# Optimization experiments

Measured on AMD Instinct MI355X. Metric: run time of the kernel, lower is better.

Reference implementation:

```python
import jax, jax.numpy as jnp
import numpy as np

LAMBDA = 0.7
RATIO = 3
EPS = 1e-6


def setup_inputs() -> dict:
    key = jax.random.key(0)
    k1, k2, k3 = jax.random.split(key, 3)
    bs, n, w, h = 8, 7, 640, 640
    preds = jax.random.normal(k1, (bs, n, w, h), dtype=jnp.float32)
    labels = jax.random.randint(k2, (bs, n, w, h), 0, 2, dtype=jnp.int32)
    training_mask = jax.random.randint(k3, (bs, w, h), 0, 2, dtype=jnp.int32)
    return {"preds": preds, "labels": labels, "training_mask": training_mask}


def _dice(S, G):
    # S, G: [C, P]; per-channel dice coefficient, then mean over channels
    num = 2.0 * jnp.sum(S * G, axis=-1)
    den = jnp.sum(S * S, axis=-1) + jnp.sum(G * G, axis=-1) + EPS
    return jnp.mean(num / den)


def _single_sample(pred, label, mask):
    # pred, label: [n, P]; mask: [P]
    P = pred.shape[-1]
    p = jax.nn.sigmoid(pred)
    pred_n = p[-1] * mask            # masked full-text prediction
    label_n = label[-1] * mask

    # --- OHEM mask M (cal_M): keep all positives + top (ratio*n_pos) hardest negatives ---
    pos = pred_n >= 0.5
    n_pos = jnp.sum(pos)
    n_neg_all = jnp.sum(~pos)
    k = n_pos * RATIO
    # sigmoid outputs are in (0,1); sentinel -1 pushes positives to the end of the descending sort
    neg_vals = jnp.where(pos, -1.0, pred_n)
    sorted_desc = -jnp.sort(-neg_vals)
    thr = sorted_desc[jnp.clip(k - 1, 0, P - 1)]  # k-th largest negative score
    ohem_active = (n_neg_all > k) & (k > 0)
    M = jnp.where(ohem_active, (pred_n >= thr).astype(jnp.float32), 1.0)

    # L_c: dice loss on OHEM-selected full-text map
    L_c = 1.0 - _dice((pred_n * M)[None, :], (label_n * M)[None, :])

    # L_s: dice loss on shrunk kernels, gated by predicted text region W
    W = (pred_n >= 0.5).astype(jnp.float32)
    L_s = 1.0 - _dice(p[:-1] * W, label[:-1] * W)

    loss = LAMBDA * L_c + (1.0 - LAMBDA) * L_s
    return L_c, L_s, loss


def reference(preds, labels, training_mask):
    bs, n, w, h = preds.shape
    preds = preds.reshape(bs, n, w * h)
    labels = labels.reshape(bs, n, w * h).astype(jnp.float32)
    mask = training_mask.reshape(bs, w * h).astype(jnp.float32)
    L_c, L_s, loss = jax.vmap(_single_sample)(preds, labels, mask)
    # reduction='mean'
    return L_c.mean(), L_s.mean(), loss.mean()
```

## Files before the change

### kernel.cpp

```cpp
#include <hip/hip_runtime.h>

#define BS   8
#define NCH  7
#define PX   409600
#define NBIN 65536
#define WIN_LO 0x3000u
#define WIN_SZ 4096
#define EPSF 1e-6f

__device__ __forceinline__ float sigf(float x) {
    return 1.0f / (1.0f + __expf(-x));
}

__device__ __forceinline__ unsigned wred_u(unsigned v) {
    #pragma unroll
    for (int o = 32; o; o >>= 1) v += __shfl_down(v, o);
    return v;
}

__device__ __forceinline__ float wred_f(float v) {
    #pragma unroll
    for (int o = 32; o; o >>= 1) v += __shfl_down(v, o);
    return v;
}

__global__ __launch_bounds__(256) void k_hist(const float* __restrict__ preds,
                                              const int* __restrict__ mask,
                                              unsigned* __restrict__ hist1,
                                              unsigned* __restrict__ n_pos) {
    int b = blockIdx.y;
    const float* pr = preds + ((size_t)b * NCH + 6) * PX;
    const int* mk = mask + (size_t)b * PX;
    __shared__ unsigned lh[WIN_SZ];
    for (int j = threadIdx.x; j < WIN_SZ; j += blockDim.x) lh[j] = 0u;
    __syncthreads();
    unsigned pos_cnt = 0, zero_cnt = 0;
    for (int i = blockIdx.x * blockDim.x + threadIdx.x; i < PX; i += gridDim.x * blockDim.x) {
        float pn = sigf(pr[i]) * (float)mk[i];
        if (pn >= 0.5f) {
            pos_cnt++;
        } else {
            unsigned bits = __float_as_uint(pn);
            if (bits == 0u) {
                zero_cnt++;
            } else {
                unsigned hb = bits >> 16;
                if (hb >= WIN_LO && hb < WIN_LO + WIN_SZ)
                    atomicAdd(&lh[hb - WIN_LO], 1u);
                else
                    atomicAdd(&hist1[(size_t)b * NBIN + hb], 1u);
            }
        }
    }
    __syncthreads();
    for (int j = threadIdx.x; j < WIN_SZ; j += blockDim.x) {
        unsigned c = lh[j];
        if (c) atomicAdd(&hist1[(size_t)b * NBIN + WIN_LO + j], c);
    }
    __shared__ unsigned ws2[2][4];
    unsigned pv = wred_u(pos_cnt), zv = wred_u(zero_cnt);
    int lane = threadIdx.x & 63, wid = threadIdx.x >> 6;
    if (lane == 0) { ws2[0][wid] = pv; ws2[1][wid] = zv; }
    __syncthreads();
    if (threadIdx.x == 0) {
        unsigned pt = 0, zt = 0;
        #pragma unroll
        for (int w = 0; w < 4; w++) { pt += ws2[0][w]; zt += ws2[1][w]; }
        if (pt) atomicAdd(&n_pos[b], pt);
        if (zt) atomicAdd(&hist1[(size_t)b * NBIN], zt);
    }
}

__device__ void select_bin(const unsigned* __restrict__ h, unsigned k,
                           unsigned* out_bin, unsigned* out_rank) {
    __shared__ unsigned cs[256];
    __shared__ unsigned sel_chunk, sel_rem;
    int t = threadIdx.x;
    unsigned s = 0;
    const unsigned* hp = h + t * 256;
    #pragma unroll 8
    for (int j = 0; j < 256; j++) s += hp[j];
    cs[t] = s;
    __syncthreads();
    #pragma unroll
    for (int off = 1; off < 256; off <<= 1) {
        unsigned v = cs[t];
        unsigned a = (t + off < 256) ? cs[t + off] : 0u;
        __syncthreads();
        cs[t] = v + a;
        __syncthreads();
    }
    {
        unsigned sfx  = cs[t];
        unsigned sfx1 = (t < 255) ? cs[t + 1] : 0u;
        if (sfx >= k && sfx1 < k) { sel_chunk = (unsigned)t; sel_rem = k - sfx1; }
    }
    __syncthreads();
    unsigned chunk = sel_chunk, krem = sel_rem;
    cs[t] = h[chunk * 256 + t];
    __syncthreads();
    #pragma unroll
    for (int off = 1; off < 256; off <<= 1) {
        unsigned v = cs[t];
        unsigned a = (t + off < 256) ? cs[t + off] : 0u;
        __syncthreads();
        cs[t] = v + a;
        __syncthreads();
    }
    {
        unsigned sfx  = cs[t];
        unsigned sfx1 = (t < 255) ? cs[t + 1] : 0u;
        if (sfx >= krem && sfx1 < krem) {
            *out_bin  = chunk * 256 + (unsigned)t;
            *out_rank = krem - sfx1;
        }
    }
    __syncthreads();
}

__global__ __launch_bounds__(256) void k_find_hi(const unsigned* __restrict__ hist1,
                                                 const unsigned* __restrict__ n_pos,
                                                 unsigned* __restrict__ hi_bin,
                                                 unsigned* __restrict__ rankv,
                                                 unsigned* __restrict__ activev,
                                                 float* __restrict__ thr) {
    int b = blockIdx.x;
    unsigned np_ = n_pos[b];
    unsigned k = np_ * 3u;
    unsigned nneg = (unsigned)PX - np_;
    if (!(nneg > k && k > 0u)) {
        if (threadIdx.x == 0) { activev[b] = 0u; thr[b] = -1.0f; }
        return;
    }
    __shared__ unsigned rb, rr;
    select_bin(hist1 + (size_t)b * NBIN, k, &rb, &rr);
    if (threadIdx.x == 0) {
        activev[b] = 1u;
        hi_bin[b] = rb;
        rankv[b] = rr;
        if (rb == 0u) thr[b] = 0.0f;
    }
}

__global__ __launch_bounds__(256) void k_refine(const float* __restrict__ preds,
                                                const int* __restrict__ mask,
                                                const unsigned* __restrict__ hi_bin,
                                                const unsigned* __restrict__ activev,
                                                unsigned* __restrict__ hist2) {
    int b = blockIdx.y;
    if (!activev[b]) return;
    unsigned hi = hi_bin[b];
    if (hi == 0u) return;
    const float* pr = preds + ((size_t)b * NCH + 6) * PX;
    const int* mk = mask + (size_t)b * PX;
    unsigned* h2 = hist2 + (size_t)b * NBIN;
    for (int i = blockIdx.x * blockDim.x + threadIdx.x; i < PX; i += gridDim.x * blockDim.x) {
        float pn = sigf(pr[i]) * (float)mk[i];
        if (pn < 0.5f) {
            unsigned bits = __float_as_uint(pn);
            if ((bits >> 16) == hi) atomicAdd(&h2[bits & 0xFFFFu], 1u);
        }
    }
}

__global__ __launch_bounds__(256) void k_find_lo(const unsigned* __restrict__ hist2,
                                                 const unsigned* __restrict__ hi_bin,
                                                 const unsigned* __restrict__ rankv,
                                                 const unsigned* __restrict__ activev,
                                                 float* __restrict__ thr) {
    int b = blockIdx.x;
    if (!activev[b]) return;
    unsigned hi = hi_bin[b];
    if (hi == 0u) return;
    __shared__ unsigned rb, rr;
    select_bin(hist2 + (size_t)b * NBIN, rankv[b], &rb, &rr);
    if (threadIdx.x == 0) thr[b] = __uint_as_float((hi << 16) | rb);
}

__global__ __launch_bounds__(256) void k_sums(const float* __restrict__ preds,
                                              const int* __restrict__ labels,
                                              const int* __restrict__ mask,
                                              const float* __restrict__ thr,
                                              float* __restrict__ sums) {
    int b = blockIdx.y;
    const float* pr = preds + (size_t)b * NCH * PX;
    const int* lb = labels + (size_t)b * NCH * PX;
    const int* mk = mask + (size_t)b * PX;
    float thr_b = thr[b];

    float a0 = 0.f, a1 = 0.f, a2 = 0.f;
    float sn[6] = {0.f, 0.f, 0.f, 0.f, 0.f, 0.f};
    float sp[6] = {0.f, 0.f, 0.f, 0.f, 0.f, 0.f};
    float sl[6] = {0.f, 0.f, 0.f, 0.f, 0.f, 0.f};

    for (int i = blockIdx.x * blockDim.x + threadIdx.x; i < PX; i += gridDim.x * blockDim.x) {
        float m  = (float)mk[i];
        float p6 = sigf(pr[6 * PX + i]);
        float pn = p6 * m;
        float Mi = (pn >= thr_b) ? 1.0f : 0.0f;
        float ln = (float)lb[6 * PX + i] * m;
        a0 += pn * ln * Mi;
        a1 += pn * pn * Mi;
        a2 += ln * Mi;
        float W = (pn >= 0.5f) ? 1.0f : 0.0f;
        #pragma unroll
        for (int c = 0; c < 6; c++) {
            float pc = sigf(pr[c * PX + i]);
            float lc = (float)lb[c * PX + i];
            sn[c] += pc * lc * W;
            sp[c] += pc * pc * W;
            sl[c] += lc * W;
        }
    }

    float vals[21];
    vals[0] = a0; vals[1] = a1; vals[2] = a2;
    #pragma unroll
    for (int c = 0; c < 6; c++) { vals[3 + c] = sn[c]; vals[9 + c] = sp[c]; vals[15 + c] = sl[c]; }

    __shared__ float red[4][21];
    int lane = threadIdx.x & 63, wid = threadIdx.x >> 6;
    #pragma unroll
    for (int j = 0; j < 21; j++) {
        float v = wred_f(vals[j]);
        if (lane == 0) red[wid][j] = v;
    }
    __syncthreads();
    if (threadIdx.x < 21) {
        float tot = red[0][threadIdx.x] + red[1][threadIdx.x] + red[2][threadIdx.x] + red[3][threadIdx.x];
        atomicAdd(&sums[b * 21 + threadIdx.x], tot);
    }
}

__global__ void k_final(const float* __restrict__ sums, float* __restrict__ out) {
    int t = threadIdx.x;
    float Lc = 0.f, Ls = 0.f;
    if (t < BS) {
        const float* s = sums + t * 21;
        Lc = 1.0f - (2.0f * s[0]) / (s[1] + s[2] + EPSF);
        float acc = 0.f;
        #pragma unroll
        for (int c = 0; c < 6; c++)
            acc += (2.0f * s[3 + c]) / (s[9 + c] + s[15 + c] + EPSF);
        Ls = 1.0f - acc * (1.0f / 6.0f);
    }
    #pragma unroll
    for (int o = 4; o; o >>= 1) { Lc += __shfl_down(Lc, o); Ls += __shfl_down(Ls, o); }
    if (t == 0) {
        float lc_m = Lc * (1.0f / (float)BS);
        float ls_m = Ls * (1.0f / (float)BS);
        out[0] = lc_m;
        out[1] = ls_m;
        out[2] = 0.7f * lc_m + 0.3f * ls_m;
    }
}

extern "C" void kernel_launch(void* const* d_in, const int* in_sizes, int n_in,
                              void* d_out, int out_size, void* d_ws, size_t ws_size,
                              hipStream_t stream) {
    const float* preds = (const float*)d_in[0];
    const int* labels  = (const int*)d_in[1];
    const int* mask    = (const int*)d_in[2];
    float* out = (float*)d_out;

    unsigned* hist1   = (unsigned*)d_ws;
    unsigned* hist2   = hist1 + (size_t)BS * NBIN;
    unsigned* n_pos   = hist2 + (size_t)BS * NBIN;
    unsigned* hi_bin  = n_pos + BS;
    unsigned* rankv   = hi_bin + BS;
    unsigned* activev = rankv + BS;
    float*    thr     = (float*)(activev + BS);
    float*    sums    = thr + BS;

    size_t zero_words = (size_t)2 * BS * NBIN + 5 * BS + (size_t)BS * 21;
    hipMemsetAsync(d_ws, 0, zero_words * sizeof(unsigned), stream);

    dim3 g1(80, BS);
    hipLaunchKernelGGL(k_hist, g1, dim3(256), 0, stream, preds, mask, hist1, n_pos);

    hipLaunchKernelGGL(k_find_hi, dim3(BS), dim3(256), 0, stream,
                       hist1, n_pos, hi_bin, rankv, activev, thr);

    dim3 g3(40, BS);
    hipLaunchKernelGGL(k_refine, g3, dim3(256), 0, stream,
                       preds, mask, hi_bin, activev, hist2);

    hipLaunchKernelGGL(k_find_lo, dim3(BS), dim3(256), 0, stream,
                       hist2, hi_bin, rankv, activev, thr);

    dim3 g5(160, BS);
    hipLaunchKernelGGL(k_sums, g5, dim3(256), 0, stream,
                       preds, labels, mask, thr, sums);

    hipLaunchKernelGGL(k_final, dim3(1), dim3(64), 0, stream, sums, out);
}
```

Measured before the change: 250.5 us.

## Fuse kernel-channel dice sums into histogram pass and add chunk-level histogram summaries

Moves the six shrunk-kernel dice accumulations, which depend only on the W>=0.5 gate, into the first histogram pass. The final pass then only reads channel 6 to apply the OHEM threshold, so the large 6-channel read no longer has to wait for threshold selection. Also keeps per-256-bin chunk counters so the select step skips the 64K-bin scan, and vectorises loads with float4/int4. The cost is extra global atomics for chunk counters in the histogram and refine passes.

```diff
diff --git a/kernel.cpp b/kernel.cpp
--- a/kernel.cpp
+++ b/kernel.cpp
@@ -4,6 +4,7 @@
 #define NCH  7
 #define PX   409600
 #define NBIN 65536
+#define NCHK 256
 #define WIN_LO 0x3000u
 #define WIN_SZ 4096
 #define EPSF 1e-6f
@@ -24,39 +25,94 @@
     return v;
 }
 
-__global__ __launch_bounds__(256) void k_hist(const float* __restrict__ preds,
+__global__ __launch_bounds__(256) void k_main(const float* __restrict__ preds,
+                                              const int* __restrict__ labels,
                                               const int* __restrict__ mask,
                                               unsigned* __restrict__ hist1,
-                                              unsigned* __restrict__ n_pos) {
+                                              unsigned* __restrict__ chunks1,
+                                              unsigned* __restrict__ n_pos,
+                                              float* __restrict__ sums) {
     int b = blockIdx.y;
-    const float* pr = preds + ((size_t)b * NCH + 6) * PX;
-    const int* mk = mask + (size_t)b * PX;
+    const float* pr = preds + (size_t)b * NCH * PX;
+    const int*   lb = labels + (size_t)b * NCH * PX;
+    const int*   mk = mask + (size_t)b * PX;
+
     __shared__ unsigned lh[WIN_SZ];
-    for (int j = threadIdx.x; j < WIN_SZ; j += blockDim.x) lh[j] = 0u;
-    __syncthreads();
+    for (int j = threadIdx.x; j < WIN_SZ; j += 256) lh[j] = 0u;
+    __syncthreads();
+
     unsigned pos_cnt = 0, zero_cnt = 0;
-    for (int i = blockIdx.x * blockDim.x + threadIdx.x; i < PX; i += gridDim.x * blockDim.x) {
-        float pn = sigf(pr[i]) * (float)mk[i];
-        if (pn >= 0.5f) {
-            pos_cnt++;
-        } else {
-            unsigned bits = __float_as_uint(pn);
-            if (bits == 0u) {
-                zero_cnt++;
+    float acc[18];
+    #pragma unroll
+    for (int j = 0; j < 18; j++) acc[j] = 0.f;
+
+    for (int g = blockIdx.x * 256 + threadIdx.x; g < PX / 4; g += gridDim.x * 256) {
+        int px = g * 4;
+        float4 p6 = *(const float4*)(pr + 6 * PX + px);
+        int4   m4 = *(const int4*)(mk + px);
+        float mm[4]  = {(float)m4.x, (float)m4.y, (float)m4.z, (float)m4.w};
+        float p6a[4] = {p6.x, p6.y, p6.z, p6.w};
+        float W[4];
+        #pragma unroll
+        for (int u = 0; u < 4; u++) {
+            float pn = sigf(p6a[u]) * mm[u];
+            if (pn >= 0.5f) {
+                pos_cnt++; W[u] = 1.0f;
             } else {
-                unsigned hb = bits >> 16;
-                if (hb >= WIN_LO && hb < WIN_LO + WIN_SZ)
-                    atomicAdd(&lh[hb - WIN_LO], 1u);
-                else
-                    atomicAdd(&hist1[(size_t)b * NBIN + hb], 1u);
+                W[u] = 0.0f;
+                unsigned bits = __float_as_uint(pn);
+                if (bits == 0u) {
+                    zero_cnt++;
+                } else {
+                    unsigned hb = bits >> 16;
+                    if (hb - WIN_LO < WIN_SZ) {
+                        atomicAdd(&lh[hb - WIN_LO], 1u);
+                    } else {
+                        atomicAdd(&hist1[(size_t)b * NBIN + hb], 1u);
+                        atomicAdd(&chunks1[b * NCHK + (hb >> 8)], 1u);
+                    }
+                }
             }
         }
-    }
-    __syncthreads();
-    for (int j = threadIdx.x; j < WIN_SZ; j += blockDim.x) {
+        #pragma unroll
+        for (int c = 0; c < 6; c++) {
+            float4 pc4 = *(const float4*)(pr + c * PX + px);
+            int4   lc4 = *(const int4*)(lb + c * PX + px);
+            float pcs[4] = {pc4.x, pc4.y, pc4.z, pc4.w};
+            float lcs[4] = {(float)lc4.x, (float)lc4.y, (float)lc4.z, (float)lc4.w};
+            #pragma unroll
+            for (int u = 0; u < 4; u++) {
+                float s = sigf(pcs[u]);
+                float l = lcs[u];
+                acc[c]      += s * l * W[u];
+                acc[6 + c]  += s * s * W[u];
+                acc[12 + c] += l * W[u];
+            }
+        }
+    }
+    __syncthreads();
+
+    for (int j = threadIdx.x; j < WIN_SZ; j += 256) {
         unsigned c = lh[j];
         if (c) atomicAdd(&hist1[(size_t)b * NBIN + WIN_LO + j], c);
     }
+    __shared__ unsigned csum[256];
+    {
+        unsigned s = 0;
+        int chunk = threadIdx.x >> 4, part = threadIdx.x & 15;
+        const unsigned* base = &lh[chunk * 256 + part * 16];
+        #pragma unroll
+        for (int j = 0; j < 16; j++) s += base[j];
+        csum[threadIdx.x] = s;
+    }
+    __syncthreads();
+    if (threadIdx.x < 16) {
+        unsigned s = 0;
+        #pragma unroll
+        for (int j = 0; j < 16; j++) s += csum[threadIdx.x * 16 + j];
+        if (s) atomicAdd(&chunks1[b * NCHK + 48 + threadIdx.x], s);
+    }
+
     __shared__ unsigned ws2[2][4];
     unsigned pv = wred_u(pos_cnt), zv = wred_u(zero_cnt);
     int lane = threadIdx.x & 63, wid = threadIdx.x >> 6;
@@ -67,20 +123,33 @@
         #pragma unroll
         for (int w = 0; w < 4; w++) { pt += ws2[0][w]; zt += ws2[1][w]; }
         if (pt) atomicAdd(&n_pos[b], pt);
-        if (zt) atomicAdd(&hist1[(size_t)b * NBIN], zt);
-    }
-}
-
-__device__ void select_bin(const unsigned* __restrict__ h, unsigned k,
-                           unsigned* out_bin, unsigned* out_rank) {
+        if (zt) {
+            atomicAdd(&hist1[(size_t)b * NBIN], zt);
+            atomicAdd(&chunks1[b * NCHK], zt);
+        }
+    }
+
+    __shared__ float red[4][18];
+    #pragma unroll
+    for (int j = 0; j < 18; j++) {
+        float v = wred_f(acc[j]);
+        if (lane == 0) red[wid][j] = v;
+    }
+    __syncthreads();
+    if (threadIdx.x < 18) {
+        float tot = red[0][threadIdx.x] + red[1][threadIdx.x] +
+                    red[2][threadIdx.x] + red[3][threadIdx.x];
+        atomicAdd(&sums[b * 21 + 3 + threadIdx.x], tot);
+    }
+}
+
+__device__ void select2(const unsigned* __restrict__ chunks,
+                        const unsigned* __restrict__ bins,
+                        unsigned k, unsigned* out_bin, unsigned* out_rank) {
     __shared__ unsigned cs[256];
-    __shared__ unsigned sel_chunk, sel_rem;
+    __shared__ unsigned sel_c, sel_r;
     int t = threadIdx.x;
-    unsigned s = 0;
-    const unsigned* hp = h + t * 256;
-    #pragma unroll 8
-    for (int j = 0; j < 256; j++) s += hp[j];
-    cs[t] = s;
+    cs[t] = chunks[t];
     __syncthreads();
     #pragma unroll
     for (int off = 1; off < 256; off <<= 1) {
@@ -93,11 +162,11 @@
     {
         unsigned sfx  = cs[t];
         unsigned sfx1 = (t < 255) ? cs[t + 1] : 0u;
-        if (sfx >= k && sfx1 < k) { sel_chunk = (unsigned)t; sel_rem = k - sfx1; }
-    }
-    __syncthreads();
-    unsigned chunk = sel_chunk, krem = sel_rem;
-    cs[t] = h[chunk * 256 + t];
+        if (sfx >= k && sfx1 < k) { sel_c = (unsigned)t; sel_r = k - sfx1; }
+    }
+    __syncthreads();
+    unsigned chunk = sel_c, krem = sel_r;
+    cs[t] = bins[chunk * 256 + t];
     __syncthreads();
     #pragma unroll
     for (int off = 1; off < 256; off <<= 1) {
@@ -119,6 +188,7 @@
 }
 
 __global__ __launch_bounds__(256) void k_find_hi(const unsigned* __restrict__ hist1,
+                                                 const unsigned* __restrict__ chunks1,
                                                  const unsigned* __restrict__ n_pos,
                                                  unsigned* __restrict__ hi_bin,
                                                  unsigned* __restrict__ rankv,
@@ -133,7 +203,7 @@
         return;
     }
     __shared__ unsigned rb, rr;
-    select_bin(hist1 + (size_t)b * NBIN, k, &rb, &rr);
+    select2(chunks1 + b * NCHK, hist1 + (size_t)b * NBIN, k, &rb, &rr);
     if (threadIdx.x == 0) {
         activev[b] = 1u;
         hi_bin[b] = rb;
@@ -146,7 +216,8 @@
                                                 const int* __restrict__ mask,
                                                 const unsigned* __restrict__ hi_bin,
                                                 const unsigned* __restrict__ activev,
-                                                unsigned* __restrict__ hist2) {
+                                                unsigned* __restrict__ hist2,
+                                                unsigned* __restrict__ chunks2) {
     int b = blockIdx.y;
     if (!activev[b]) return;
     unsigned hi = hi_bin[b];
@@ -154,16 +225,30 @@
     const float* pr = preds + ((size_t)b * NCH + 6) * PX;
     const int* mk = mask + (size_t)b * PX;
     unsigned* h2 = hist2 + (size_t)b * NBIN;
-    for (int i = blockIdx.x * blockDim.x + threadIdx.x; i < PX; i += gridDim.x * blockDim.x) {
-        float pn = sigf(pr[i]) * (float)mk[i];
-        if (pn < 0.5f) {
-            unsigned bits = __float_as_uint(pn);
-            if ((bits >> 16) == hi) atomicAdd(&h2[bits & 0xFFFFu], 1u);
+    unsigned* c2 = chunks2 + b * NCHK;
+    for (int g = blockIdx.x * 256 + threadIdx.x; g < PX / 4; g += gridDim.x * 256) {
+        int px = g * 4;
+        float4 p6 = *(const float4*)(pr + px);
+        int4   m4 = *(const int4*)(mk + px);
+        float p6a[4] = {p6.x, p6.y, p6.z, p6.w};
+        float mm[4]  = {(float)m4.x, (float)m4.y, (float)m4.z, (float)m4.w};
+        #pragma unroll
+        for (int u = 0; u < 4; u++) {
+            float pn = sigf(p6a[u]) * mm[u];
+            if (pn < 0.5f) {
+                unsigned bits = __float_as_uint(pn);
+                if ((bits >> 16) == hi) {
+                    unsigned lo = bits & 0xFFFFu;
+                    atomicAdd(&h2[lo], 1u);
+                    atomicAdd(&c2[lo >> 8], 1u);
+                }
+            }
         }
     }
 }
 
 __global__ __launch_bounds__(256) void k_find_lo(const unsigned* __restrict__ hist2,
+                                                 const unsigned* __restrict__ chunks2,
                                                  const unsigned* __restrict__ hi_bin,
                                                  const unsigned* __restrict__ rankv,
                                                  const unsigned* __restrict__ activev,
@@ -173,61 +258,48 @@
     unsigned hi = hi_bin[b];
     if (hi == 0u) return;
     __shared__ unsigned rb, rr;
-    select_bin(hist2 + (size_t)b * NBIN, rankv[b], &rb, &rr);
+    select2(chunks2 + b * NCHK, hist2 + (size_t)b * NBIN, rankv[b], &rb, &rr);
     if (threadIdx.x == 0) thr[b] = __uint_as_float((hi << 16) | rb);
 }
 
-__global__ __launch_bounds__(256) void k_sums(const float* __restrict__ preds,
-                                              const int* __restrict__ labels,
-                                              const int* __restrict__ mask,
-                                              const float* __restrict__ thr,
-                                              float* __restrict__ sums) {
+__global__ __launch_bounds__(256) void k_lc(const float* __restrict__ preds,
+                                            const int* __restrict__ labels,
+                                            const int* __restrict__ mask,
+                                            const float* __restrict__ thr,
+                                            float* __restrict__ sums) {
     int b = blockIdx.y;
-    const float* pr = preds + (size_t)b * NCH * PX;
-    const int* lb = labels + (size_t)b * NCH * PX;
-    const int* mk = mask + (size_t)b * PX;
+    const float* pr = preds + ((size_t)b * NCH + 6) * PX;
+    const int*   lb = labels + ((size_t)b * NCH + 6) * PX;
+    const int*   mk = mask + (size_t)b * PX;
     float thr_b = thr[b];
 
     float a0 = 0.f, a1 = 0.f, a2 = 0.f;
-    float sn[6] = {0.f, 0.f, 0.f, 0.f, 0.f, 0.f};
-    float sp[6] = {0.f, 0.f, 0.f, 0.f, 0.f, 0.f};
-    float sl[6] = {0.f, 0.f, 0.f, 0.f, 0.f, 0.f};
-
-    for (int i = blockIdx.x * blockDim.x + threadIdx.x; i < PX; i += gridDim.x * blockDim.x) {
-        float m  = (float)mk[i];
-        float p6 = sigf(pr[6 * PX + i]);
-        float pn = p6 * m;
-        float Mi = (pn >= thr_b) ? 1.0f : 0.0f;
-        float ln = (float)lb[6 * PX + i] * m;
-        a0 += pn * ln * Mi;
-        a1 += pn * pn * Mi;
-        a2 += ln * Mi;
-        float W = (pn >= 0.5f) ? 1.0f : 0.0f;
-        #pragma unroll
-        for (int c = 0; c < 6; c++) {
-            float pc = sigf(pr[c * PX + i]);
-            float lc = (float)lb[c * PX + i];
-            sn[c] += pc * lc * W;
-            sp[c] += pc * pc * W;
-            sl[c] += lc * W;
-        }
-    }
-
-    float vals[21];
-    vals[0] = a0; vals[1] = a1; vals[2] = a2;
-    #pragma unroll
-    for (int c = 0; c < 6; c++) { vals[3 + c] = sn[c]; vals[9 + c] = sp[c]; vals[15 + c] = sl[c]; }
-
-    __shared__ float red[4][21];
+    for (int g = blockIdx.x * 256 + threadIdx.x; g < PX / 4; g += gridDim.x * 256) {
+        int px = g * 4;
+        float4 p6 = *(const float4*)(pr + px);
+        int4   l4 = *(const int4*)(lb + px);
+        int4   m4 = *(const int4*)(mk + px);
+        float p6a[4] = {p6.x, p6.y, p6.z, p6.w};
+        float la[4]  = {(float)l4.x, (float)l4.y, (float)l4.z, (float)l4.w};
+        float mm[4]  = {(float)m4.x, (float)m4.y, (float)m4.z, (float)m4.w};
+        #pragma unroll
+        for (int u = 0; u < 4; u++) {
+            float pn = sigf(p6a[u]) * mm[u];
+            float Mi = (pn >= thr_b) ? 1.0f : 0.0f;
+            float ln = la[u] * mm[u];
+            a0 += pn * ln * Mi;
+            a1 += pn * pn * Mi;
+            a2 += ln * Mi;
+        }
+    }
+    __shared__ float red[4][3];
     int lane = threadIdx.x & 63, wid = threadIdx.x >> 6;
-    #pragma unroll
-    for (int j = 0; j < 21; j++) {
-        float v = wred_f(vals[j]);
-        if (lane == 0) red[wid][j] = v;
-    }
-    __syncthreads();
-    if (threadIdx.x < 21) {
-        float tot = red[0][threadIdx.x] + red[1][threadIdx.x] + red[2][threadIdx.x] + red[3][threadIdx.x];
+    float v0 = wred_f(a0), v1 = wred_f(a1), v2 = wred_f(a2);
+    if (lane == 0) { red[wid][0] = v0; red[wid][1] = v1; red[wid][2] = v2; }
+    __syncthreads();
+    if (threadIdx.x < 3) {
+        float tot = red[0][threadIdx.x] + red[1][threadIdx.x] +
+                    red[2][threadIdx.x] + red[3][threadIdx.x];
         atomicAdd(&sums[b * 21 + threadIdx.x], tot);
     }
 }
@@ -265,31 +337,31 @@
 
     unsigned* hist1   = (unsigned*)d_ws;
     unsigned* hist2   = hist1 + (size_t)BS * NBIN;
-    unsigned* n_pos   = hist2 + (size_t)BS * NBIN;
+    unsigned* chunks1 = hist2 + (size_t)BS * NBIN;
+    unsigned* chunks2 = chunks1 + (size_t)BS * NCHK;
+    unsigned* n_pos   = chunks2 + (size_t)BS * NCHK;
     unsigned* hi_bin  = n_pos + BS;
     unsigned* rankv   = hi_bin + BS;
     unsigned* activev = rankv + BS;
     float*    thr     = (float*)(activev + BS);
     float*    sums    = thr + BS;
 
-    size_t zero_words = (size_t)2 * BS * NBIN + 5 * BS + (size_t)BS * 21;
+    size_t zero_words = (size_t)2 * BS * NBIN + (size_t)2 * BS * NCHK + 5 * BS + (size_t)BS * 21;
     hipMemsetAsync(d_ws, 0, zero_words * sizeof(unsigned), stream);
 
-    dim3 g1(80, BS);
-    hipLaunchKernelGGL(k_hist, g1, dim3(256), 0, stream, preds, mask, hist1, n_pos);
+    hipLaunchKernelGGL(k_main, dim3(100, BS), dim3(256), 0, stream,
+                       preds, labels, mask, hist1, chunks1, n_pos, sums);
 
     hipLaunchKernelGGL(k_find_hi, dim3(BS), dim3(256), 0, stream,
-                       hist1, n_pos, hi_bin, rankv, activev, thr);
-
-    dim3 g3(40, BS);
-    hipLaunchKernelGGL(k_refine, g3, dim3(256), 0, stream,
-                       preds, mask, hi_bin, activev, hist2);
+                       hist1, chunks1, n_pos, hi_bin, rankv, activev, thr);
+
+    hipLaunchKernelGGL(k_refine, dim3(32, BS), dim3(256), 0, stream,
+                       preds, mask, hi_bin, activev, hist2, chunks2);
 
     hipLaunchKernelGGL(k_find_lo, dim3(BS), dim3(256), 0, stream,
-                       hist2, hi_bin, rankv, activev, thr);
-
-    dim3 g5(160, BS);
-    hipLaunchKernelGGL(k_sums, g5, dim3(256), 0, stream,
+                       hist2, chunks2, hi_bin, rankv, activev, thr);
+
+    hipLaunchKernelGGL(k_lc, dim3(100, BS), dim3(256), 0, stream,
                        preds, labels, mask, thr, sums);
 
     hipLaunchKernelGGL(k_final, dim3(1), dim3(64), 0, stream, sums, out);
```

Result: faster. 233.0 us (-7.0%).
